# Kernel tuning notes

Hardware: AMD Instinct MI355X
Metric: run time of the kernel (lower is better)

## Reference

```python
import jax, jax.numpy as jnp
import numpy as np

B, C, H, W = 1, 512, 64, 64
HEADS, DIM_HEAD = 8, 64
GROUPS = 32
EPS = 1e-5
SCALE = DIM_HEAD ** -0.5


def setup_inputs() -> dict:
    key = jax.random.key(0)
    ks = jax.random.split(key, 8)
    inner = HEADS * DIM_HEAD  # 512
    s = 0.02
    return {
        "hidden_states": jax.random.normal(ks[0], (B, C, H, W), jnp.float32),
        "gn_gamma": jnp.ones((C,), jnp.float32),
        "gn_beta": jnp.zeros((C,), jnp.float32),
        "wq": jax.random.normal(ks[1], (inner, C), jnp.float32) * s,
        "wk": jax.random.normal(ks[2], (inner, C), jnp.float32) * s,
        "wv": jax.random.normal(ks[3], (inner, C), jnp.float32) * s,
        "wo": jax.random.normal(ks[4], (C, inner), jnp.float32) * s,
        "bo": jnp.zeros((C,), jnp.float32),
    }


def _group_norm(x, gamma, beta):
    # x: [B, C, H, W]; normalize within channel groups over (C//G, H, W)
    b, c, h, w = x.shape
    xg = x.reshape(b, GROUPS, c // GROUPS, h, w)
    mean = xg.mean(axis=(2, 3, 4), keepdims=True)
    var = xg.var(axis=(2, 3, 4), keepdims=True)
    xg = (xg - mean) * jax.lax.rsqrt(var + EPS)
    x = xg.reshape(b, c, h, w)
    return x * gamma[None, :, None, None] + beta[None, :, None, None]


def reference(hidden_states, gn_gamma, gn_beta, wq, wk, wv, wo, bo):
    residual = hidden_states
    x = _group_norm(hidden_states, gn_gamma, gn_beta)
    b, c, h, w = x.shape
    n = h * w
    x = x.reshape(b, c, n).transpose(0, 2, 1)  # [B, N, C]

    # torch Linear: y = x @ W^T (bias=False for q/k/v)
    q = (x @ wq.T).reshape(b, n, HEADS, DIM_HEAD).transpose(0, 2, 1, 3)  # [B,H,N,D]
    k = (x @ wk.T).reshape(b, n, HEADS, DIM_HEAD).transpose(0, 2, 1, 3)
    v = (x @ wv.T).reshape(b, n, HEADS, DIM_HEAD).transpose(0, 2, 1, 3)

    scores = jnp.einsum("bhqd,bhkd->bhqk", q, k) * SCALE  # [B,H,N,N]
    probs = jax.nn.softmax(scores, axis=-1)
    out = jnp.einsum("bhqk,bhkd->bhqd", probs, v)  # [B,H,N,D]

    out = out.transpose(0, 2, 1, 3).reshape(b, n, HEADS * DIM_HEAD)  # [B,N,inner]
    out = out @ wo.T + bo  # [B,N,C]
    out = out.transpose(0, 2, 1).reshape(b, c, h, w)
    return out + residual
```

## Files before the change

kernel.cpp:

```cpp
#include <hip/hip_runtime.h>

#define N_TOK 4096
#define C_DIM 512
#define NH    8
#define EPS   1e-5f
#define NSPLIT 4
#define THR   11.0f

typedef __attribute__((ext_vector_type(8))) __bf16 bf16x8;
typedef __attribute__((ext_vector_type(4))) float  f32x4;
using u16 = unsigned short;
using u32 = unsigned int;

#define MFMA16 __builtin_amdgcn_mfma_f32_16x16x32_bf16

__device__ __forceinline__ u16 f2bf(float f){
  u32 x = __builtin_bit_cast(u32, f);
  x += 0x7fffu + ((x>>16)&1u);
  return (u16)(x>>16);
}
__device__ __forceinline__ float bf2f(u16 v){
  return __builtin_bit_cast(float, (u32)v<<16);
}
__device__ __forceinline__ float exp2a(float x){
  float r; asm("v_exp_f32 %0, %1" : "=v"(r) : "v"(x)); return r;
}
__device__ __forceinline__ u32 cvtpk(float lo, float hi){
  u32 r; asm("v_cvt_pk_bf16_f32 %0, %1, %2" : "=v"(r) : "v"(lo), "v"(hi)); return r;
}
__device__ __forceinline__ float max3a(float a, float b, float c){
  float r; asm("v_max3_f32 %0, %1, %2, %3" : "=v"(r) : "v"(a), "v"(b), "v"(c)); return r;
}
__device__ __forceinline__ void dma16(const void* src, void* lds){
  __builtin_amdgcn_global_load_lds(
      (const __attribute__((address_space(1))) u32*)src,
      (__attribute__((address_space(3))) u32*)lds, 16, 0, 0);
}

__global__ __launch_bounds__(256) void k_pre(const float* __restrict__ s0,
      const float* __restrict__ s1, const float* __restrict__ s2,
      const float* __restrict__ s3, u16* __restrict__ d0, u16* __restrict__ d1,
      u16* __restrict__ d2, u16* __restrict__ d3,
      const float* __restrict__ x, float* __restrict__ pstat){
  __shared__ float rs[4], rss[4];
  int b = blockIdx.x;
  if (b < 1024){
    int m = b >> 8;
    int i = (b & 255)*256 + threadIdx.x;
    const float* s = m==0?s0 : m==1?s1 : m==2?s2 : s3;
    u16*         d = m==0?d0 : m==1?d1 : m==2?d2 : d3;
    float4 v = ((const float4*)s)[i];
    ushort4 o; o.x=f2bf(v.x); o.y=f2bf(v.y); o.z=f2bf(v.z); o.w=f2bf(v.w);
    ((ushort4*)d)[i] = o;
    return;
  }
  int gb = b - 1024;
  int g = gb>>3, p = gb&7, t = threadIdx.x;
  const float4* gx4 = (const float4*)(x + (size_t)g*16*N_TOK) + (size_t)p*2048;
  float s=0.f, ss=0.f;
  #pragma unroll
  for (int k=0;k<8;k++){
    float4 v = gx4[t + k*256];
    s  += v.x+v.y+v.z+v.w;
    ss += v.x*v.x+v.y*v.y+v.z*v.z+v.w*v.w;
  }
  for (int m=1;m<64;m<<=1){ s += __shfl_xor(s,m); ss += __shfl_xor(ss,m); }
  int w=t>>6, lane=t&63;
  if (lane==0){ rs[w]=s; rss[w]=ss; }
  __syncthreads();
  if (t==0){
    pstat[(g*8+p)*2  ] = rs[0]+rs[1]+rs[2]+rs[3];
    pstat[(g*8+p)*2+1] = rss[0]+rss[1]+rss[2]+rss[3];
  }
}

__global__ __launch_bounds__(256) void k_gn_apply(const float* __restrict__ x,
      const float* __restrict__ pstat, const float* __restrict__ gamma,
      const float* __restrict__ beta, u16* __restrict__ X){
  int g = blockIdx.x, c0 = g*16;
  int n = blockIdx.y*256 + threadIdx.x;
  float S=0.f, SS=0.f;
  #pragma unroll
  for (int p=0;p<8;p++){ S += pstat[(g*8+p)*2]; SS += pstat[(g*8+p)*2+1]; }
  float mean = S*(1.f/65536.f);
  float rstd = rsqrtf(SS*(1.f/65536.f) - mean*mean + EPS);
  u16 ov[16];
  #pragma unroll
  for (int c=0;c<16;c++){
    float gm = gamma[c0+c]*rstd;
    float be = beta[c0+c] - mean*gm;
    float v  = x[(size_t)(c0+c)*N_TOK + n]*gm + be;
    ov[c] = f2bf(v);
  }
  uint4* dst = (uint4*)&X[(size_t)n*C_DIM + c0];
  dst[0] = *(uint4*)&ov[0];
  dst[1] = *(uint4*)&ov[8];
}

__device__ __forceinline__ void gemm_core(const u16* A, const u16* B,
      int m0, int n0, char* LDS, f32x4 (&acc)[4][4]){
  int t = threadIdx.x, w = t>>6, l = t&63, lr = l&15, li = l>>4;
  int wr = w>>1, wc = w&1;
  char* As = LDS;
  char* Bs = LDS + 32768;
  const char* Ac = (const char*)A;
  const char* Bc = (const char*)B;
  int ys   = ((l&7)*16) ^ ((l>>3)<<4);
  int rswz = (lr&7)<<4;

  size_t arow[4], brow[4]; int ldst[4];
  #pragma unroll
  for (int r=0;r<4;r++){
    int row = w*32 + r*8 + (l>>3);
    arow[r] = (size_t)(m0+row)*1024 + ys;
    brow[r] = (size_t)(n0+row)*1024 + ys;
    ldst[r] = w*4096 + r*1024;
  }
  #pragma unroll
  for (int r=0;r<4;r++){
    dma16(Ac + arow[r], As + ldst[r]);
    dma16(Bc + brow[r], Bs + ldst[r]);
  }
  __syncthreads();

  int buf = 0;
  for (int it=0; it<8; it++){
    if (it < 7){
      int nb = buf^1;
      #pragma unroll
      for (int r=0;r<4;r++){
        dma16(Ac + arow[r] + (it+1)*128, As + nb*16384 + ldst[r]);
        dma16(Bc + brow[r] + (it+1)*128, Bs + nb*16384 + ldst[r]);
      }
    }
    char* Ab = As + buf*16384;
    char* Bb = Bs + buf*16384;
    #pragma unroll
    for (int ks=0; ks<2; ks++){
      bf16x8 af[4], bfr[4];
      #pragma unroll
      for (int i=0;i<4;i++){
        int rowA = wr*64 + i*16 + lr;
        int rowB = wc*64 + i*16 + lr;
        af[i]  = *(const bf16x8*)(Ab + rowA*128 + ((li*16 + ks*64) ^ rswz));
        bfr[i] = *(const bf16x8*)(Bb + rowB*128 + ((li*16 + ks*64) ^ rswz));
      }
      __builtin_amdgcn_s_setprio(1);
      #pragma unroll
      for (int i=0;i<4;i++){
        #pragma unroll
        for (int j=0;j<4;j++){
          acc[i][j] = MFMA16(af[i], bfr[j], acc[i][j], 0,0,0);
        }
      }
      __builtin_amdgcn_s_setprio(0);
    }
    __syncthreads();
    buf ^= 1;
  }
}

__global__ __launch_bounds__(256,2) void k_qkv2(const u16* __restrict__ X,
      const u16* __restrict__ wq, const u16* __restrict__ wk,
      const u16* __restrict__ wv, u16* __restrict__ Qo, u16* __restrict__ Ko,
      u16* __restrict__ Vto){
  __shared__ char LDS[65536];
  int b = blockIdx.x;
  const u16 *A, *B; u16* Cp; int ldc, m0, n0; float sc = 1.f; bool vperm = false;
  if (b < 128){        A=X;  B=wq; Cp=Qo;  ldc=512;  m0=(b>>2)*128; n0=(b&3)*128;
                       sc = 0.125f*1.44269504f; }
  else if (b < 256){ int r=b-128; A=X;  B=wk; Cp=Ko;  ldc=512;  m0=(r>>2)*128; n0=(r&3)*128; }
  else             { int r=b-256; A=wv; B=X;  Cp=Vto; ldc=4096; m0=(r>>5)*128; n0=(r&31)*128;
                     vperm = true; }

  f32x4 acc[4][4] = {};
  gemm_core(A, B, m0, n0, LDS, acc);

  int t = threadIdx.x, w = t>>6, l = t&63, lr = l&15, li = l>>4;
  int wr = w>>1, wc = w&1;
  #pragma unroll
  for (int i=0;i<4;i++){
    #pragma unroll
    for (int rr=0;rr<4;rr++){
      int mm = m0 + wr*64 + i*16 + li*4 + rr;
      #pragma unroll
      for (int j=0;j<4;j++){
        int nn = n0 + wc*64 + j*16 + lr;
        if (vperm){
          int tl = nn & 63;
          int pos = (tl & 35) | ((tl & 12) << 1) | ((tl & 16) >> 2);
          nn = (nn & ~63) | pos;
        }
        Cp[(size_t)mm*ldc + nn] = f2bf(acc[i][j][rr]*sc);
      }
    }
  }
}

__global__ __launch_bounds__(256,2) void k_oproj2(const u16* __restrict__ Wo,
      const u16* __restrict__ Ob, const float* __restrict__ bo,
      const float* __restrict__ res, float* __restrict__ out){
  __shared__ char LDS[65536];
  int r0 = blockIdx.x;
  int m0 = (r0>>5)*128, n0 = (r0&31)*128;

  f32x4 acc[4][4] = {};
  gemm_core(Wo, Ob, m0, n0, LDS, acc);

  int t = threadIdx.x, w = t>>6, l = t&63, lr = l&15, li = l>>4;
  int wr = w>>1, wc = w&1;
  #pragma unroll
  for (int i=0;i<4;i++){
    #pragma unroll
    for (int rr=0;rr<4;rr++){
      int cc = m0 + wr*64 + i*16 + li*4 + rr;
      float bias = bo[cc];
      #pragma unroll
      for (int j=0;j<4;j++){
        int nn = n0 + wc*64 + j*16 + lr;
        size_t off = (size_t)cc*4096 + nn;
        out[off] = acc[i][j][rr] + bias + res[off];
      }
    }
  }
}

__global__ __launch_bounds__(256,4) void k_attn6(const u16* __restrict__ Q,
      const u16* __restrict__ K, const u16* __restrict__ Vt,
      u16* __restrict__ Opart, float* __restrict__ ml){
  __shared__ char KV[2][16384];
  int h = blockIdx.y, sp = blockIdx.z;
  int q0 = blockIdx.x*128;
  int t = threadIdx.x, w = t>>6, l = t&63, lr = l&15, li = l>>4;
  char* KVb = (char*)KV;
  int qbase = q0 + w*32;

  const u16* Qp = Q + (size_t)(qbase + lr)*512 + h*64 + li*8;
  bf16x8 qa00 = *(const bf16x8*)(Qp);
  bf16x8 qa01 = *(const bf16x8*)(Qp + 32);
  bf16x8 qa10 = *(const bf16x8*)(Qp + 16*512);
  bf16x8 qa11 = *(const bf16x8*)(Qp + 16*512 + 32);

  int srow = l>>3, y0 = (l&7)*16;
  const char* Kc = (const char*)K;
  const char* Vc = (const char*)Vt;
  const char* ksrc[2]; const char* vsrc[2]; int ldso[2];
  #pragma unroll
  for (int j=0;j<2;j++){
    int row = w*16 + j*8 + srow;
    int ys  = y0 ^ ((row&7)<<4);
    ksrc[j] = Kc + (size_t)(sp*1024 + row)*1024 + h*128 + ys;
    vsrc[j] = Vc + (size_t)(h*64 + row)*8192 + sp*2048 + ys;
    ldso[j] = w*2048 + j*1024;
  }

  #pragma unroll
  for (int j=0;j<2;j++){
    dma16(ksrc[j], KVb + ldso[j]);
    dma16(vsrc[j], KVb + 8192 + ldso[j]);
  }
  __syncthreads();

  f32x4 acc0[4] = {}; f32x4 acc1[4] = {};
  float m0=-1e30f, m1=-1e30f, l0=0.f, l1=0.f;
  int buf = 0;

  for (int it=0; it<16; it++){
    if (it < 15){
      int nb = buf^1;
      #pragma unroll
      for (int j=0;j<2;j++){
        dma16(ksrc[j] + (size_t)(it+1)*65536, KVb + nb*16384 + ldso[j]);
        dma16(vsrc[j] + (it+1)*128,           KVb + nb*16384 + 8192 + ldso[j]);
      }
    }
    char* Klb = KVb + buf*16384;
    char* Vlb = Klb + 8192;

    f32x4 st0[4] = {}; f32x4 st1[4] = {};
    __builtin_amdgcn_s_setprio(1);
    #pragma unroll
    for (int T=0;T<4;T++){
      int row = T*16 + lr, swz = (row&7)<<4;
      const char* rb = Klb + row*128;
      bf16x8 k0 = *(const bf16x8*)(rb + ((li*16     ) ^ swz));
      bf16x8 k1 = *(const bf16x8*)(rb + ((li*16 + 64) ^ swz));
      st0[T] = MFMA16(k0, qa00, st0[T], 0,0,0);
      st0[T] = MFMA16(k1, qa01, st0[T], 0,0,0);
      st1[T] = MFMA16(k0, qa10, st1[T], 0,0,0);
      st1[T] = MFMA16(k1, qa11, st1[T], 0,0,0);
    }
    __builtin_amdgcn_s_setprio(0);

    u32 pk0[8], pk1[8];
    {
      float a0 = max3a(st0[0][0],st0[0][1],st0[0][2]);
      float a1 = max3a(st0[1][0],st0[1][1],st0[1][2]);
      float a2 = max3a(st0[2][0],st0[2][1],st0[2][2]);
      float a3 = max3a(st0[3][0],st0[3][1],st0[3][2]);
      float b0 = max3a(st0[0][3],st0[1][3],st0[2][3]);
      float pmax = fmaxf(max3a(a0,a1,a2), max3a(a3,b0,st0[3][3]));
      pmax = fmaxf(pmax, __shfl_xor(pmax,16));
      pmax = fmaxf(pmax, __shfl_xor(pmax,32));
      if (!__all(pmax <= m0 + THR)){
        float mnew = fmaxf(m0, pmax);
        float fac = exp2a(m0 - mnew);
        m0 = mnew; l0 *= fac;
        float f0=__shfl(fac, li*20+0), f1=__shfl(fac, li*20+1);
        float f2=__shfl(fac, li*20+2), f3=__shfl(fac, li*20+3);
        #pragma unroll
        for (int T=0;T<4;T++){
          acc0[T][0]*=f0; acc0[T][1]*=f1; acc0[T][2]*=f2; acc0[T][3]*=f3;
        }
      }
      float lad = 0.f;
      #pragma unroll
      for (int T=0;T<4;T++){
        float p0=exp2a(st0[T][0]-m0), p1=exp2a(st0[T][1]-m0);
        float p2=exp2a(st0[T][2]-m0), p3=exp2a(st0[T][3]-m0);
        lad += (p0+p1)+(p2+p3);
        pk0[T*2]   = cvtpk(p0,p1);
        pk0[T*2+1] = cvtpk(p2,p3);
      }
      l0 += lad;
    }
    {
      float a0 = max3a(st1[0][0],st1[0][1],st1[0][2]);
      float a1 = max3a(st1[1][0],st1[1][1],st1[1][2]);
      float a2 = max3a(st1[2][0],st1[2][1],st1[2][2]);
      float a3 = max3a(st1[3][0],st1[3][1],st1[3][2]);
      float b0 = max3a(st1[0][3],st1[1][3],st1[2][3]);
      float pmax = fmaxf(max3a(a0,a1,a2), max3a(a3,b0,st1[3][3]));
      pmax = fmaxf(pmax, __shfl_xor(pmax,16));
      pmax = fmaxf(pmax, __shfl_xor(pmax,32));
      if (!__all(pmax <= m1 + THR)){
        float mnew = fmaxf(m1, pmax);
        float fac = exp2a(m1 - mnew);
        m1 = mnew; l1 *= fac;
        float f0=__shfl(fac, li*20+0), f1=__shfl(fac, li*20+1);
        float f2=__shfl(fac, li*20+2), f3=__shfl(fac, li*20+3);
        #pragma unroll
        for (int T=0;T<4;T++){
          acc1[T][0]*=f0; acc1[T][1]*=f1; acc1[T][2]*=f2; acc1[T][3]*=f3;
        }
      }
      float lad = 0.f;
      #pragma unroll
      for (int T=0;T<4;T++){
        float p0=exp2a(st1[T][0]-m1), p1=exp2a(st1[T][1]-m1);
        float p2=exp2a(st1[T][2]-m1), p3=exp2a(st1[T][3]-m1);
        lad += (p0+p1)+(p2+p3);
        pk1[T*2]   = cvtpk(p0,p1);
        pk1[T*2+1] = cvtpk(p2,p3);
      }
      l1 += lad;
    }

    __builtin_amdgcn_s_setprio(1);
    #pragma unroll
    for (int c=0;c<2;c++){
      union { bf16x8 v; u32 u[4]; } A0, A1;
      #pragma unroll
      for (int k=0;k<4;k++){ A0.u[k]=pk0[c*4+k]; A1.u[k]=pk1[c*4+k]; }
      #pragma unroll
      for (int T=0;T<4;T++){
        int vrow = T*16 + lr, vswz = (vrow&7)<<4;
        bf16x8 vb = *(const bf16x8*)(Vlb + vrow*128 + ((c*64 + li*16) ^ vswz));
        acc0[T] = MFMA16(A0.v, vb, acc0[T], 0,0,0);
        acc1[T] = MFMA16(A1.v, vb, acc1[T], 0,0,0);
      }
    }
    __builtin_amdgcn_s_setprio(0);

    __syncthreads();
    buf ^= 1;
  }

  l0 += __shfl_xor(l0,16); l0 += __shfl_xor(l0,32);
  l1 += __shfl_xor(l1,16); l1 += __shfl_xor(l1,32);
  u16* Op = Opart + (size_t)sp*N_TOK*C_DIM;
  #pragma unroll
  for (int T=0;T<4;T++){
    #pragma unroll
    for (int r=0;r<4;r++){
      Op[(size_t)(qbase      + li*4 + r)*512 + h*64 + T*16 + lr] = f2bf(acc0[T][r]);
      Op[(size_t)(qbase + 16 + li*4 + r)*512 + h*64 + T*16 + lr] = f2bf(acc1[T][r]);
    }
  }
  if (li==0){
    float* p0 = ml + (((size_t)sp*NH + h)*N_TOK + qbase + lr)*2;
    p0[0]=m0; p0[1]=l0;
    float* p1 = ml + (((size_t)sp*NH + h)*N_TOK + qbase + 16 + lr)*2;
    p1[0]=m1; p1[1]=l1;
  }
}

__global__ __launch_bounds__(256) void k_merge2(const u16* __restrict__ Opart,
      const float* __restrict__ ml, u16* __restrict__ Ob){
  int i  = blockIdx.x*256 + threadIdx.x;
  int q  = i >> 7;
  int c4 = i & 127;
  int h  = c4 >> 4;
  float m[NSPLIT], lv[NSPLIT];
  #pragma unroll
  for (int s=0;s<NSPLIT;s++){
    const float* p = ml + (((size_t)s*NH + h)*N_TOK + q)*2;
    m[s]=p[0]; lv[s]=p[1];
  }
  float M = fmaxf(max3a(m[0],m[1],m[2]), m[3]);
  float wgt[NSPLIT]; float L = 0.f;
  #pragma unroll
  for (int s=0;s<NSPLIT;s++){ wgt[s] = exp2a(m[s]-M); L += lv[s]*wgt[s]; }
  float inv = 1.f/L;
  float4 o = {0.f,0.f,0.f,0.f};
  #pragma unroll
  for (int s=0;s<NSPLIT;s++){
    ushort4 a = ((const ushort4*)(Opart + (size_t)s*N_TOK*C_DIM))[i];
    o.x += bf2f(a.x)*wgt[s]; o.y += bf2f(a.y)*wgt[s];
    o.z += bf2f(a.z)*wgt[s]; o.w += bf2f(a.w)*wgt[s];
  }
  ushort4 r;
  r.x=f2bf(o.x*inv); r.y=f2bf(o.y*inv); r.z=f2bf(o.z*inv); r.w=f2bf(o.w*inv);
  ((ushort4*)Ob)[i] = r;
}

extern "C" void kernel_launch(void* const* d_in, const int* in_sizes, int n_in,
                              void* d_out, int out_size, void* d_ws, size_t ws_size,
                              hipStream_t stream){
  (void)in_sizes; (void)n_in; (void)out_size; (void)ws_size;
  const float* hs    = (const float*)d_in[0];
  const float* gamma = (const float*)d_in[1];
  const float* beta  = (const float*)d_in[2];
  const float* wq    = (const float*)d_in[3];
  const float* wk    = (const float*)d_in[4];
  const float* wv    = (const float*)d_in[5];
  const float* wo    = (const float*)d_in[6];
  const float* bo    = (const float*)d_in[7];
  float* out = (float*)d_out;

  u16* X   = (u16*)d_ws;
  u16* Qb  = X   + (size_t)4096*512;
  u16* Kb  = Qb  + (size_t)4096*512;
  u16* Vtb = Kb  + (size_t)4096*512;
  u16* Ob  = Vtb + (size_t)4096*512;
  u16* wqb = Ob  + (size_t)4096*512;
  u16* wkb = wqb + (size_t)512*512;
  u16* wvb = wkb + (size_t)512*512;
  u16* wob = wvb + (size_t)512*512;
  float* pstat = (float*)(wob + (size_t)512*512);
  u16* Opart   = (u16*)(pstat + 1024);
  float* mlbuf = (float*)(Opart + (size_t)NSPLIT*4096*512);

  k_pre<<<1280,256,0,stream>>>(wq, wk, wv, wo, wqb, wkb, wvb, wob, hs, pstat);
  dim3 ga(32, 16);
  k_gn_apply<<<ga,256,0,stream>>>(hs, pstat, gamma, beta, X);
  k_qkv2<<<384,256,0,stream>>>(X, wqb, wkb, wvb, Qb, Kb, Vtb);
  dim3 gat(32, 8, NSPLIT);
  k_attn6<<<gat,256,0,stream>>>(Qb, Kb, Vtb, Opart, mlbuf);
  k_merge2<<<2048,256,0,stream>>>(Opart, mlbuf, Ob);
  k_oproj2<<<128,256,0,stream>>>(wob, Ob, bo, hs, out);
}
```

Measured before the change: 85.99 us.

## Shrink GEMM tiles to 128x64 and double attention KV split count

The QKV and output-projection GEMMs move from 128x128 to 128x64 tiles with a new staging loader, smaller LDS and higher occupancy bounds. That doubles their block counts, so the 256-CU device is better filled (the output projection previously launched only 128 blocks). Attention flash-decoding splits go from 4 to 8, which gives 1024 blocks with half the KV loop each. In exchange there is more partial-output traffic and more merge work, and the GEMMs get less data reuse per tile.

```diff
diff --git a/kernel.cpp b/kernel.cpp
--- a/kernel.cpp
+++ b/kernel.cpp
@@ -4,7 +4,7 @@
 #define C_DIM 512
 #define NH    8
 #define EPS   1e-5f
-#define NSPLIT 4
+#define NSPLIT 8
 #define THR   11.0f
 
 typedef __attribute__((ext_vector_type(8))) __bf16 bf16x8;
@@ -97,59 +97,62 @@
   dst[1] = *(uint4*)&ov[8];
 }
 
-__device__ __forceinline__ void gemm_core(const u16* A, const u16* B,
-      int m0, int n0, char* LDS, f32x4 (&acc)[4][4]){
+__device__ __forceinline__ void gemm_core64(const u16* A, const u16* B,
+      int m0, int n0, char* LDS, f32x4 (&acc)[4][2]){
   int t = threadIdx.x, w = t>>6, l = t&63, lr = l&15, li = l>>4;
   int wr = w>>1, wc = w&1;
   char* As = LDS;
   char* Bs = LDS + 32768;
-  const char* Ac = (const char*)A;
-  const char* Bc = (const char*)B;
-  int ys   = ((l&7)*16) ^ ((l>>3)<<4);
+  const char* Ac = (const char*)A + (size_t)m0*1024;
+  const char* Bc = (const char*)B + (size_t)n0*1024;
   int rswz = (lr&7)<<4;
 
-  size_t arow[4], brow[4]; int ldst[4];
-  #pragma unroll
-  for (int r=0;r<4;r++){
-    int row = w*32 + r*8 + (l>>3);
-    arow[r] = (size_t)(m0+row)*1024 + ys;
-    brow[r] = (size_t)(n0+row)*1024 + ys;
-    ldst[r] = w*4096 + r*1024;
-  }
-  #pragma unroll
-  for (int r=0;r<4;r++){
-    dma16(Ac + arow[r], As + ldst[r]);
-    dma16(Bc + brow[r], Bs + ldst[r]);
-  }
+  int rowA[4], segA[4], rowB[2], segB[2];
+  #pragma unroll
+  for (int k=0;k<4;k++){ int s=t+k*256; rowA[k]=s>>3; segA[k]=s&7; }
+  #pragma unroll
+  for (int k=0;k<2;k++){ int s=t+k*256; rowB[k]=s>>3; segB[k]=s&7; }
+
+  #define STAGE(it, bb) { int koff=(it)*128;                                   \
+    _Pragma("unroll")                                                          \
+    for (int k=0;k<4;k++){                                                     \
+      int ys = (segA[k]*16) ^ ((rowA[k]&7)<<4);                                \
+      dma16(Ac + (size_t)rowA[k]*1024 + koff + ys,                             \
+            As + (bb)*16384 + w*1024 + k*4096);                                \
+    }                                                                          \
+    _Pragma("unroll")                                                          \
+    for (int k=0;k<2;k++){                                                     \
+      int ys = (segB[k]*16) ^ ((rowB[k]&7)<<4);                                \
+      dma16(Bc + (size_t)rowB[k]*1024 + koff + ys,                             \
+            Bs + (bb)*8192 + w*1024 + k*4096);                                 \
+    } }
+
+  STAGE(0, 0);
   __syncthreads();
 
   int buf = 0;
   for (int it=0; it<8; it++){
-    if (it < 7){
-      int nb = buf^1;
-      #pragma unroll
-      for (int r=0;r<4;r++){
-        dma16(Ac + arow[r] + (it+1)*128, As + nb*16384 + ldst[r]);
-        dma16(Bc + brow[r] + (it+1)*128, Bs + nb*16384 + ldst[r]);
-      }
-    }
+    if (it < 7){ STAGE(it+1, buf^1); }
     char* Ab = As + buf*16384;
-    char* Bb = Bs + buf*16384;
+    char* Bb = Bs + buf*8192;
     #pragma unroll
     for (int ks=0; ks<2; ks++){
-      bf16x8 af[4], bfr[4];
+      bf16x8 af[4], bfr[2];
       #pragma unroll
       for (int i=0;i<4;i++){
-        int rowA = wr*64 + i*16 + lr;
-        int rowB = wc*64 + i*16 + lr;
-        af[i]  = *(const bf16x8*)(Ab + rowA*128 + ((li*16 + ks*64) ^ rswz));
-        bfr[i] = *(const bf16x8*)(Bb + rowB*128 + ((li*16 + ks*64) ^ rswz));
+        int ra = wr*64 + i*16 + lr;
+        af[i]  = *(const bf16x8*)(Ab + ra*128 + ((li*16 + ks*64) ^ rswz));
+      }
+      #pragma unroll
+      for (int j=0;j<2;j++){
+        int rb = wc*32 + j*16 + lr;
+        bfr[j] = *(const bf16x8*)(Bb + rb*128 + ((li*16 + ks*64) ^ rswz));
       }
       __builtin_amdgcn_s_setprio(1);
       #pragma unroll
       for (int i=0;i<4;i++){
         #pragma unroll
-        for (int j=0;j<4;j++){
+        for (int j=0;j<2;j++){
           acc[i][j] = MFMA16(af[i], bfr[j], acc[i][j], 0,0,0);
         }
       }
@@ -158,23 +161,24 @@
     __syncthreads();
     buf ^= 1;
   }
-}
-
-__global__ __launch_bounds__(256,2) void k_qkv2(const u16* __restrict__ X,
+  #undef STAGE
+}
+
+__global__ __launch_bounds__(256,3) void k_qkv2(const u16* __restrict__ X,
       const u16* __restrict__ wq, const u16* __restrict__ wk,
       const u16* __restrict__ wv, u16* __restrict__ Qo, u16* __restrict__ Ko,
       u16* __restrict__ Vto){
-  __shared__ char LDS[65536];
+  __shared__ char LDS[49152];
   int b = blockIdx.x;
   const u16 *A, *B; u16* Cp; int ldc, m0, n0; float sc = 1.f; bool vperm = false;
-  if (b < 128){        A=X;  B=wq; Cp=Qo;  ldc=512;  m0=(b>>2)*128; n0=(b&3)*128;
+  if (b < 256){        A=X;  B=wq; Cp=Qo;  ldc=512;  m0=(b>>3)*128; n0=(b&7)*64;
                        sc = 0.125f*1.44269504f; }
-  else if (b < 256){ int r=b-128; A=X;  B=wk; Cp=Ko;  ldc=512;  m0=(r>>2)*128; n0=(r&3)*128; }
-  else             { int r=b-256; A=wv; B=X;  Cp=Vto; ldc=4096; m0=(r>>5)*128; n0=(r&31)*128;
+  else if (b < 512){ int r=b-256; A=X;  B=wk; Cp=Ko;  ldc=512;  m0=(r>>3)*128; n0=(r&7)*64; }
+  else             { int r=b-512; A=wv; B=X;  Cp=Vto; ldc=4096; m0=(r>>6)*128; n0=(r&63)*64;
                      vperm = true; }
 
-  f32x4 acc[4][4] = {};
-  gemm_core(A, B, m0, n0, LDS, acc);
+  f32x4 acc[4][2] = {};
+  gemm_core64(A, B, m0, n0, LDS, acc);
 
   int t = threadIdx.x, w = t>>6, l = t&63, lr = l&15, li = l>>4;
   int wr = w>>1, wc = w&1;
@@ -184,8 +188,8 @@
     for (int rr=0;rr<4;rr++){
       int mm = m0 + wr*64 + i*16 + li*4 + rr;
       #pragma unroll
-      for (int j=0;j<4;j++){
-        int nn = n0 + wc*64 + j*16 + lr;
+      for (int j=0;j<2;j++){
+        int nn = n0 + wc*32 + j*16 + lr;
         if (vperm){
           int tl = nn & 63;
           int pos = (tl & 35) | ((tl & 12) << 1) | ((tl & 16) >> 2);
@@ -197,15 +201,15 @@
   }
 }
 
-__global__ __launch_bounds__(256,2) void k_oproj2(const u16* __restrict__ Wo,
+__global__ __launch_bounds__(256,3) void k_oproj2(const u16* __restrict__ Wo,
       const u16* __restrict__ Ob, const float* __restrict__ bo,
       const float* __restrict__ res, float* __restrict__ out){
-  __shared__ char LDS[65536];
-  int r0 = blockIdx.x;
-  int m0 = (r0>>5)*128, n0 = (r0&31)*128;
-
-  f32x4 acc[4][4] = {};
-  gemm_core(Wo, Ob, m0, n0, LDS, acc);
+  __shared__ char LDS[49152];
+  int b = blockIdx.x;
+  int m0 = (b>>6)*128, n0 = (b&63)*64;
+
+  f32x4 acc[4][2] = {};
+  gemm_core64(Wo, Ob, m0, n0, LDS, acc);
 
   int t = threadIdx.x, w = t>>6, l = t&63, lr = l&15, li = l>>4;
   int wr = w>>1, wc = w&1;
@@ -216,8 +220,8 @@
       int cc = m0 + wr*64 + i*16 + li*4 + rr;
       float bias = bo[cc];
       #pragma unroll
-      for (int j=0;j<4;j++){
-        int nn = n0 + wc*64 + j*16 + lr;
+      for (int j=0;j<2;j++){
+        int nn = n0 + wc*32 + j*16 + lr;
         size_t off = (size_t)cc*4096 + nn;
         out[off] = acc[i][j][rr] + bias + res[off];
       }
@@ -225,7 +229,7 @@
   }
 }
 
-__global__ __launch_bounds__(256,4) void k_attn6(const u16* __restrict__ Q,
+__global__ __launch_bounds__(256,5) void k_attn6(const u16* __restrict__ Q,
       const u16* __restrict__ K, const u16* __restrict__ Vt,
       u16* __restrict__ Opart, float* __restrict__ ml){
   __shared__ char KV[2][16384];
@@ -249,8 +253,8 @@
   for (int j=0;j<2;j++){
     int row = w*16 + j*8 + srow;
     int ys  = y0 ^ ((row&7)<<4);
-    ksrc[j] = Kc + (size_t)(sp*1024 + row)*1024 + h*128 + ys;
-    vsrc[j] = Vc + (size_t)(h*64 + row)*8192 + sp*2048 + ys;
+    ksrc[j] = Kc + (size_t)(sp*512 + row)*1024 + h*128 + ys;
+    vsrc[j] = Vc + (size_t)(h*64 + row)*8192 + sp*1024 + ys;
     ldso[j] = w*2048 + j*1024;
   }
 
@@ -265,8 +269,8 @@
   float m0=-1e30f, m1=-1e30f, l0=0.f, l1=0.f;
   int buf = 0;
 
-  for (int it=0; it<16; it++){
-    if (it < 15){
+  for (int it=0; it<8; it++){
+    if (it < 7){
       int nb = buf^1;
       #pragma unroll
       for (int j=0;j<2;j++){
@@ -407,7 +411,8 @@
     const float* p = ml + (((size_t)s*NH + h)*N_TOK + q)*2;
     m[s]=p[0]; lv[s]=p[1];
   }
-  float M = fmaxf(max3a(m[0],m[1],m[2]), m[3]);
+  float M = fmaxf(fmaxf(max3a(m[0],m[1],m[2]), max3a(m[3],m[4],m[5])),
+                  fmaxf(m[6],m[7]));
   float wgt[NSPLIT]; float L = 0.f;
   #pragma unroll
   for (int s=0;s<NSPLIT;s++){ wgt[s] = exp2a(m[s]-M); L += lv[s]*wgt[s]; }
@@ -454,9 +459,9 @@
   k_pre<<<1280,256,0,stream>>>(wq, wk, wv, wo, wqb, wkb, wvb, wob, hs, pstat);
   dim3 ga(32, 16);
   k_gn_apply<<<ga,256,0,stream>>>(hs, pstat, gamma, beta, X);
-  k_qkv2<<<384,256,0,stream>>>(X, wqb, wkb, wvb, Qb, Kb, Vtb);
+  k_qkv2<<<768,256,0,stream>>>(X, wqb, wkb, wvb, Qb, Kb, Vtb);
   dim3 gat(32, 8, NSPLIT);
   k_attn6<<<gat,256,0,stream>>>(Qb, Kb, Vtb, Opart, mlbuf);
   k_merge2<<<2048,256,0,stream>>>(Opart, mlbuf, Ob);
-  k_oproj2<<<128,256,0,stream>>>(wob, Ob, bo, hs, out);
-}
+  k_oproj2<<<256,256,0,stream>>>(wob, Ob, bo, hs, out);
+}
```

Result: slower. 169.5 us (+97.1%).
